# Optimization experiments

Hardware: AMD Instinct MI355X
Metric: run time of the kernel (lower is better)

## Reference

```python
import jax, jax.numpy as jnp
import numpy as np

HEADS, DIM_HEAD = 8, 96
DIM = HEADS * DIM_HEAD            # 768
DEPTH = 8
MEM_LAYERS = (4, 5)               # layers with KNN-retrieval attention
TOPK = 32                         # num_retrieved_memories
CLIP_LEN, PREFIX_LEN = 10, 10
NEG = -1e9


def layernorm(x, g, b):
    m = x.mean(-1, keepdims=True)
    v = ((x - m) ** 2).mean(-1, keepdims=True)
    return (x - m) * jax.lax.rsqrt(v + 1e-5) * g + b


def attention(x, wq_l, wkv_l, wo_l, mem_k=None, mem_v=None):
    # one-headed key/values (memorizing-transformers style), multi-head queries
    b, n, _ = x.shape
    q = (x @ wq_l).reshape(b, n, HEADS, DIM_HEAD).transpose(0, 2, 1, 3)  # [b,h,n,d]
    q = q * (DIM_HEAD ** -0.5)
    kv = x @ wkv_l                                   # [b,n,2d]
    k, v = kv[..., :DIM_HEAD], kv[..., DIM_HEAD:]    # [b,n,d] each
    sim = jnp.einsum('bhid,bjd->bhij', q, k)         # local scores
    causal = jnp.tril(jnp.ones((n, n), dtype=bool))
    sim = jnp.where(causal, sim, NEG)
    if mem_k is not None:
        # exact inner-product top-k retrieval from per-batch memory bank
        mem_sim = jnp.einsum('bhid,bmd->bhim', q, mem_k)      # [b,h,n,M]
        top_sim, top_idx = jax.lax.top_k(mem_sim, TOPK)       # [b,h,n,K]
        mem_v_sel = jnp.take_along_axis(
            mem_v[:, None, None], top_idx[..., None], axis=3)  # [b,h,n,K,d]
        attn = jax.nn.softmax(jnp.concatenate([top_sim, sim], axis=-1), axis=-1)
        mem_attn, loc_attn = attn[..., :TOPK], attn[..., TOPK:]
        out = (jnp.einsum('bhij,bhijd->bhid', mem_attn, mem_v_sel)
               + jnp.einsum('bhij,bjd->bhid', loc_attn, v))
    else:
        attn = jax.nn.softmax(sim, axis=-1)
        out = jnp.einsum('bhij,bjd->bhid', attn, v)
    out = out.transpose(0, 2, 1, 3).reshape(b, n, DIM)
    return out @ wo_l


def setup_inputs() -> dict:
    key = jax.random.key(0)
    ks = jax.random.split(key, 12)
    s = 0.02
    inp = {
        'x': jax.random.normal(ks[0], (16, 640), jnp.float32),
        'linear_w': jax.random.normal(ks[1], (640, CLIP_LEN * DIM), jnp.float32) * s,
        'linear_b': jnp.zeros((CLIP_LEN * DIM,), jnp.float32),
        'prefix_const': jax.random.normal(ks[2], (PREFIX_LEN, DIM), jnp.float32),
        'ln1_g': jnp.ones((DEPTH, DIM), jnp.float32),
        'ln1_b': jnp.zeros((DEPTH, DIM), jnp.float32),
        'wq': jax.random.normal(ks[3], (DEPTH, DIM, DIM), jnp.float32) * s,
        'wkv': jax.random.normal(ks[4], (DEPTH, DIM, 2 * DIM_HEAD), jnp.float32) * s,
        'wo': jax.random.normal(ks[5], (DEPTH, DIM, DIM), jnp.float32) * s,
        'ln2_g': jnp.ones((DEPTH, DIM), jnp.float32),
        'ln2_b': jnp.zeros((DEPTH, DIM), jnp.float32),
        'w1': jax.random.normal(ks[6], (DEPTH, DIM, 4 * DIM), jnp.float32) * s,
        'b1': jnp.zeros((DEPTH, 4 * DIM), jnp.float32),
        'w2': jax.random.normal(ks[7], (DEPTH, 4 * DIM, DIM), jnp.float32) * s,
        'b2': jnp.zeros((DEPTH, DIM), jnp.float32),
        'lnf_g': jnp.ones((DIM,), jnp.float32),
        'lnf_b': jnp.zeros((DIM,), jnp.float32),
        'mem_k': jax.random.normal(ks[8], (16, 32768, DIM_HEAD), jnp.float32),
        'mem_v': jax.random.normal(ks[9], (16, 32768, DIM_HEAD), jnp.float32),
    }
    return inp


def reference(x, linear_w, linear_b, prefix_const,
              ln1_g, ln1_b, wq, wkv, wo, ln2_g, ln2_b,
              w1, b1, w2, b2, lnf_g, lnf_b, mem_k, mem_v):
    b = x.shape[0]
    # linear projection of clip feature -> clip_length tokens
    h = (x @ linear_w + linear_b).reshape(b, CLIP_LEN, DIM)
    prefix = jnp.broadcast_to(prefix_const[None], (b, PREFIX_LEN, DIM))
    t = jnp.concatenate([h, prefix], axis=1)  # [b, 20, dim]
    for l in range(DEPTH):
        mk, mv = (mem_k, mem_v) if l in MEM_LAYERS else (None, None)
        t = t + attention(layernorm(t, ln1_g[l], ln1_b[l]), wq[l], wkv[l], wo[l], mk, mv)
        hf = layernorm(t, ln2_g[l], ln2_b[l])
        t = t + (jax.nn.gelu(hf @ w1[l] + b1[l]) @ w2[l] + b2[l])
    t = layernorm(t, lnf_g, lnf_b)
    return t[:, CLIP_LEN:]  # [b, prefix_length, dim]
```

## Files before the change

### kernel.cpp

```cpp
#include <hip/hip_runtime.h>
#include <hip/hip_bf16.h>

#define BB 16
#define NSEQ 20
#define HEADS 8
#define DH 96
#define DIM 768
#define FF 3072
#define KMEM 32768
#define NCHUNK 8
#define CHUNK 4096
#define CAP 128

typedef unsigned short u16;
typedef __attribute__((ext_vector_type(8))) short short8v;
typedef __attribute__((ext_vector_type(4))) float f32x4;

__device__ __forceinline__ u16 f2bu(float x) {
    __hip_bfloat16 h = __float2bfloat16(x);
    return *reinterpret_cast<u16*>(&h);
}

__global__ __launch_bounds__(256) void conv_k(const float* __restrict__ src, u16* __restrict__ dst, int n)
{
    int i = blockIdx.x * 256 + threadIdx.x;
    if (i < n) dst[i] = f2bu(src[i]);
}

__device__ __forceinline__ void tconv_tile(const float* __restrict__ src, u16* __restrict__ dst,
                                           int K, int N, int kt, int nt, int tx, int ty)
{
    __shared__ float tile[32][33];
    int k0 = kt * 32, n0 = nt * 32;
#pragma unroll
    for (int i = 0; i < 4; i++)
        tile[ty + 8 * i][tx] = src[(size_t)(k0 + ty + 8 * i) * N + n0 + tx];
    __syncthreads();
#pragma unroll
    for (int i = 0; i < 4; i++)
        dst[(size_t)(n0 + ty + 8 * i) * K + k0 + tx] = f2bu(tile[tx][ty + 8 * i]);
}

__global__ __launch_bounds__(256) void tconv_k(const float* __restrict__ src, u16* __restrict__ dst, int K, int N)
{
    int tilesN = N >> 5;
    tconv_tile(src, dst, K, N, blockIdx.x / tilesN, blockIdx.x % tilesN,
               threadIdx.x & 31, threadIdx.x >> 5);
}

__global__ __launch_bounds__(256) void wconv5_k(const float* __restrict__ wq, const float* __restrict__ wkv,
    const float* __restrict__ wo, const float* __restrict__ w1, const float* __restrict__ w2,
    u16* __restrict__ wt)
{
    int bx = blockIdx.x;
    int tx = threadIdx.x & 31, ty = threadIdx.x >> 5;
    if (bx < 576)       tconv_tile(wq,  wt + 0,       768, 768,  bx / 24,          bx % 24,          tx, ty);
    else if (bx < 720)  tconv_tile(wkv, wt + 589824,  768, 192,  (bx - 576) / 6,   (bx - 576) % 6,   tx, ty);
    else if (bx < 1296) tconv_tile(wo,  wt + 737280,  768, 768,  (bx - 720) / 24,  (bx - 720) % 24,  tx, ty);
    else if (bx < 3600) tconv_tile(w1,  wt + 1327104, 768, 3072, (bx - 1296) / 96, (bx - 1296) % 96, tx, ty);
    else                tconv_tile(w2,  wt + 3686400, 3072, 768, (bx - 3600) / 24, (bx - 3600) % 24, tx, ty);
}

__device__ __forceinline__ void storeC(float* C, size_t idx, float v) { C[idx] = v; }
__device__ __forceinline__ void storeC(u16* C, size_t idx, float v)   { C[idx] = f2bu(v); }

template <typename CT>
__global__ __launch_bounds__(256) void gemm_bt(const u16* __restrict__ A, const u16* __restrict__ Bt,
    const float* __restrict__ bias, const float* __restrict__ resid, CT* __restrict__ C,
    int M, int N, int K, int lda, int ldc, float scale, int act)
{
    int tid = threadIdx.x;
    int w = tid >> 6, lane = tid & 63;
    int m0 = blockIdx.y * 16;
    int n0 = blockIdx.x * 128 + w * 32;
    int row = lane & 15;
    int kg  = lane >> 4;
    const u16* arow = A + (size_t)(m0 + row) * lda + kg * 8;
    int c0 = n0 + row;
    int c1 = n0 + 16 + row;
    const u16* bt0 = Bt + (size_t)min(c0, N - 1) * K + kg * 8;
    const u16* bt1 = Bt + (size_t)min(c1, N - 1) * K + kg * 8;
    f32x4 acc0 = {0.f, 0.f, 0.f, 0.f};
    f32x4 acc1 = {0.f, 0.f, 0.f, 0.f};
#pragma unroll 2
    for (int k0 = 0; k0 < K; k0 += 32) {
        short8v af = *(const short8v*)(arow + k0);
        short8v b0 = *(const short8v*)(bt0 + k0);
        short8v b1 = *(const short8v*)(bt1 + k0);
        acc0 = __builtin_amdgcn_mfma_f32_16x16x32_bf16(af, b0, acc0, 0, 0, 0);
        acc1 = __builtin_amdgcn_mfma_f32_16x16x32_bf16(af, b1, acc1, 0, 0, 0);
    }
#pragma unroll
    for (int r = 0; r < 4; r++) {
        int rw = m0 + kg * 4 + r;
        if (c0 < N) {
            float v = acc0[r] * scale;
            if (bias) v += bias[c0];
            if (act) {
                float xx = v;
                float tt = 0.7978845608028654f * (xx + 0.044715f * xx * xx * xx);
                v = 0.5f * xx * (1.0f + tanhf(tt));
            }
            if (resid) v += resid[(size_t)rw * ldc + c0];
            storeC(C, (size_t)rw * ldc + c0, v);
        }
        if (c1 < N) {
            float v = acc1[r] * scale;
            if (bias) v += bias[c1];
            if (act) {
                float xx = v;
                float tt = 0.7978845608028654f * (xx + 0.044715f * xx * xx * xx);
                v = 0.5f * xx * (1.0f + tanhf(tt));
            }
            if (resid) v += resid[(size_t)rw * ldc + c1];
            storeC(C, (size_t)rw * ldc + c1, v);
        }
    }
}

__global__ __launch_bounds__(256) void ln_k(const float* __restrict__ x, const float* __restrict__ g,
    const float* __restrict__ bb, u16* __restrict__ y)
{
    int row = blockIdx.x;
    const float* xr = x + (size_t)row * DIM;
    int tid = threadIdx.x;
    float v0 = xr[tid], v1 = xr[tid + 256], v2 = xr[tid + 512];
    __shared__ float red[4];
    float s = v0 + v1 + v2;
    for (int off = 32; off; off >>= 1) s += __shfl_down(s, off);
    if ((tid & 63) == 0) red[tid >> 6] = s;
    __syncthreads();
    float mean = (red[0] + red[1] + red[2] + red[3]) * (1.f / 768.f);
    __syncthreads();
    float d0 = v0 - mean, d1 = v1 - mean, d2 = v2 - mean;
    s = d0 * d0 + d1 * d1 + d2 * d2;
    for (int off = 32; off; off >>= 1) s += __shfl_down(s, off);
    if ((tid & 63) == 0) red[tid >> 6] = s;
    __syncthreads();
    float var = (red[0] + red[1] + red[2] + red[3]) * (1.f / 768.f);
    float rs = rsqrtf(var + 1e-5f);
    u16* yr = y + (size_t)row * DIM;
    yr[tid]       = f2bu(d0 * rs * g[tid]       + bb[tid]);
    yr[tid + 256] = f2bu(d1 * rs * g[tid + 256] + bb[tid + 256]);
    yr[tid + 512] = f2bu(d2 * rs * g[tid + 512] + bb[tid + 512]);
}

__global__ __launch_bounds__(256) void lnf_k(const float* __restrict__ x, const float* __restrict__ g,
    const float* __restrict__ bb, float* __restrict__ out)
{
    int blk = blockIdx.x;
    int b = blk / 10, ii = blk - b * 10;
    int row = b * NSEQ + 10 + ii;
    const float* xr = x + (size_t)row * DIM;
    int tid = threadIdx.x;
    float v0 = xr[tid], v1 = xr[tid + 256], v2 = xr[tid + 512];
    __shared__ float red[4];
    float s = v0 + v1 + v2;
    for (int off = 32; off; off >>= 1) s += __shfl_down(s, off);
    if ((tid & 63) == 0) red[tid >> 6] = s;
    __syncthreads();
    float mean = (red[0] + red[1] + red[2] + red[3]) * (1.f / 768.f);
    __syncthreads();
    float d0 = v0 - mean, d1 = v1 - mean, d2 = v2 - mean;
    s = d0 * d0 + d1 * d1 + d2 * d2;
    for (int off = 32; off; off >>= 1) s += __shfl_down(s, off);
    if ((tid & 63) == 0) red[tid >> 6] = s;
    __syncthreads();
    float var = (red[0] + red[1] + red[2] + red[3]) * (1.f / 768.f);
    float rs = rsqrtf(var + 1e-5f);
    float* orow = out + ((size_t)(b * 10 + ii)) * DIM;
    orow[tid]       = d0 * rs * g[tid]       + bb[tid];
    orow[tid + 256] = d1 * rs * g[tid + 256] + bb[tid + 256];
    orow[tid + 512] = d2 * rs * g[tid + 512] + bb[tid + 512];
}

__global__ __launch_bounds__(256) void prefix_k(const float* __restrict__ p, float* __restrict__ t)
{
    int idx = blockIdx.x * 256 + threadIdx.x;
    if (idx < BB * 7680) {
        int b = idx / 7680;
        int r = idx - b * 7680;
        t[(size_t)b * (NSEQ * DIM) + 7680 + r] = p[r];
    }
}

__global__ __launch_bounds__(256) void lattn_k(const float* __restrict__ q, const float* __restrict__ kv,
    u16* __restrict__ ao)
{
    int b = blockIdx.x, h = blockIdx.y;
    __shared__ float sims[NSEQ][NSEQ];
    __shared__ float probs[NSEQ][NSEQ];
    const float* qb = q + (size_t)b * NSEQ * DIM + h * DH;
    const float* kb = kv + (size_t)b * NSEQ * 192;
    int tid = threadIdx.x;
    for (int p = tid; p < NSEQ * NSEQ; p += 256) {
        int i = p / NSEQ, j = p - i * NSEQ;
        float s;
        if (j > i) s = -1.0e9f;
        else {
            s = 0.f;
            for (int d = 0; d < DH; d++) s = fmaf(qb[(size_t)i * DIM + d], kb[j * 192 + d], s);
        }
        sims[i][j] = s;
    }
    __syncthreads();
    if (tid < NSEQ) {
        int i = tid;
        float m = -1e30f;
        for (int j = 0; j < NSEQ; j++) m = fmaxf(m, sims[i][j]);
        float sum = 0.f;
        for (int j = 0; j < NSEQ; j++) { float e = expf(sims[i][j] - m); probs[i][j] = e; sum += e; }
        float inv = 1.f / sum;
        for (int j = 0; j < NSEQ; j++) probs[i][j] *= inv;
    }
    __syncthreads();
    for (int p = tid; p < NSEQ * DH; p += 256) {
        int i = p / DH, d = p - i * DH;
        float o = 0.f;
        for (int j = 0; j <= i; j++) o = fmaf(probs[i][j], kb[j * 192 + 96 + d], o);
        ao[((size_t)b * NSEQ + i) * DIM + h * DH + d] = f2bu(o);
    }
}

__device__ __forceinline__ bool tk_better(float va, int ia, float vb, int ib) {
    return (va > vb) || (va == vb && ia < ib);
}

__device__ __forceinline__ void lds_fence() {
    asm volatile("s_waitcnt lgkmcnt(0)" ::: "memory");
    __builtin_amdgcn_sched_barrier(0);
}

__device__ void topk32(float* bv, int* bi, int cnt, int lane,
                       float& ov, int& oi, float& thr_out) {
    lds_fence();
    float v0 = (lane < cnt)      ? bv[lane]      : -3.0e38f;
    int   i0 = (lane < cnt)      ? bi[lane]      : 0x7fffffff;
    float v1 = (lane + 64 < cnt) ? bv[lane + 64] : -3.0e38f;
    int   i1 = (lane + 64 < cnt) ? bi[lane + 64] : 0x7fffffff;
    lds_fence();
#pragma unroll
    for (int k = 2; k <= 128; k <<= 1) {
#pragma unroll
        for (int j = 64; j >= 1; j >>= 1) {
            if (j >= k) continue;
            if (j == 64) {
                bool asc = ((lane & k) == 0);
                bool b01 = tk_better(v0, i0, v1, i1);
                if (b01 != asc) { float tv = v0; int ti = i0; v0 = v1; i0 = i1; v1 = tv; i1 = ti; }
            } else {
                {
                    float pv = __shfl_xor(v0, j); int pi = __shfl_xor(i0, j);
                    bool asc = ((lane & k) == 0);
                    bool first = ((lane & j) == 0);
                    bool mb = tk_better(v0, i0, pv, pi);
                    bool keep = first ? (mb == asc) : (mb != asc);
                    if (!keep) { v0 = pv; i0 = pi; }
                }
                {
                    float pv = __shfl_xor(v1, j); int pi = __shfl_xor(i1, j);
                    bool asc = (((lane + 64) & k) == 0);
                    bool first = ((lane & j) == 0);
                    bool mb = tk_better(v1, i1, pv, pi);
                    bool keep = first ? (mb == asc) : (mb != asc);
                    if (!keep) { v1 = pv; i1 = pi; }
                }
            }
        }
    }
    if (lane < 32) { bv[lane] = v0; bi[lane] = i0; }
    lds_fence();
    ov = v0; oi = i0;
    thr_out = __shfl(v0, 31);
}

__device__ __forceinline__ void tk_pass(const float4 kr[6], const float4 qreg[5][6],
    float thrR[5], int cntR[5], float (*bufv)[CAP], int (*bufi)[CAP],
    int r0, int lane, int qt, int key)
{
    float a[5];
#pragma unroll
    for (int rr = 0; rr < 5; rr++) a[rr] = 0.f;
#pragma unroll
    for (int i = 0; i < 6; i++) {
        float4 kv = kr[i];
#pragma unroll
        for (int rr = 0; rr < 5; rr++) {
            float4 qv = qreg[rr][i];
            a[rr] = fmaf(qv.x, kv.x, a[rr]);
            a[rr] = fmaf(qv.y, kv.y, a[rr]);
            a[rr] = fmaf(qv.z, kv.z, a[rr]);
            a[rr] = fmaf(qv.w, kv.w, a[rr]);
        }
    }
#pragma unroll
    for (int rr = 0; rr < 5; rr++) {
        a[rr] += __shfl_xor(a[rr], 1);
        a[rr] += __shfl_xor(a[rr], 2);
    }
#pragma unroll
    for (int rr = 0; rr < 5; rr++) {
        bool cand = (qt == 0) && (a[rr] >= thrR[rr]);
        unsigned long long mask = __ballot(cand);
        int n = __popcll(mask);
        if (n) {
            int r = r0 + rr;
            if (cntR[rr] + n > CAP) {
                float dv; int di;
                topk32(&bufv[r][0], &bufi[r][0], cntR[rr], lane, dv, di, thrR[rr]);
                cntR[rr] = 32;
            }
            int pos = cntR[rr] + __popcll(mask & ((1ull << lane) - 1ull));
            if (cand) { bufv[r][pos] = a[rr]; bufi[r][pos] = key; }
            cntR[rr] += n;
        }
    }
}

__global__ __launch_bounds__(256, 2) void memtopk_k(const float* __restrict__ q, const float* __restrict__ memk,
    float* __restrict__ tkv, int* __restrict__ tki)
{
    __shared__ float bufv[NSEQ][CAP];
    __shared__ int   bufi[NSEQ][CAP];
    int c = blockIdx.x, h = blockIdx.y, b = blockIdx.z;
    int tid = threadIdx.x;
    int lane = tid & 63;
    int w = tid >> 6;
    int r0 = w * 5;
    int qt = lane & 3;
    int kk = lane >> 2;

    float4 qreg[5][6];
#pragma unroll
    for (int rr = 0; rr < 5; rr++) {
        const float4* qrow = (const float4*)(q + ((size_t)(b * NSEQ + r0 + rr)) * DIM + h * DH + qt * 24);
#pragma unroll
        for (int i = 0; i < 6; i++) qreg[rr][i] = qrow[i];
    }

    float thrR[5]; int cntR[5];
#pragma unroll
    for (int rr = 0; rr < 5; rr++) { thrR[rr] = -3.0e38f; cntR[rr] = 0; }

    const float* kbase = memk + (size_t)b * KMEM * DH;
    int k0 = c * CHUNK;

    float4 ka[6], kb2[6];
    {
        const float4* kp = (const float4*)(kbase + (size_t)(k0 + kk) * DH + qt * 24);
#pragma unroll
        for (int i = 0; i < 6; i++) ka[i] = kp[i];
    }
    for (int p = 0; p < CHUNK / 16; p += 2) {
        int key0 = k0 + p * 16 + kk;
        {
            const float4* kp = (const float4*)(kbase + (size_t)(key0 + 16) * DH + qt * 24);
#pragma unroll
            for (int i = 0; i < 6; i++) kb2[i] = kp[i];
        }
        tk_pass(ka, qreg, thrR, cntR, bufv, bufi, r0, lane, qt, key0);
        if (p + 2 < CHUNK / 16) {
            const float4* kp = (const float4*)(kbase + (size_t)(key0 + 32) * DH + qt * 24);
#pragma unroll
            for (int i = 0; i < 6; i++) ka[i] = kp[i];
        }
        tk_pass(kb2, qreg, thrR, cntR, bufv, bufi, r0, lane, qt, key0 + 16);
    }
#pragma unroll
    for (int rr = 0; rr < 5; rr++) {
        int r = r0 + rr;
        float ov; int oi; float dthr;
        topk32(&bufv[r][0], &bufi[r][0], cntR[rr], lane, ov, oi, dthr);
        if (lane < 32) {
            size_t base = ((((size_t)b * HEADS + h) * NSEQ + r) * NCHUNK + c) * 32;
            tkv[base + lane] = ov;
            tki[base + lane] = oi;
        }
    }
}

__global__ __launch_bounds__(64) void memattn_k(const float* __restrict__ q, const float* __restrict__ kv,
    const float* __restrict__ memv, const float* __restrict__ tkv, const int* __restrict__ tki,
    u16* __restrict__ ao)
{
    int i = blockIdx.x, h = blockIdx.y, b = blockIdx.z;
    __shared__ float cv[NCHUNK * 32];
    __shared__ int   ci[NCHUNK * 32];
    __shared__ float selv[32];
    __shared__ int   seli[32];
    __shared__ float ls[NSEQ];
    __shared__ float probs[52];
    int tid = threadIdx.x;
    size_t base = (((size_t)b * HEADS + h) * NSEQ + i) * (NCHUNK * 32);
#pragma unroll
    for (int s = 0; s < NCHUNK * 32 / 64; s++) {
        cv[tid + 64 * s] = tkv[base + tid + 64 * s];
        ci[tid + 64 * s] = tki[base + tid + 64 * s];
    }
    const float* qr = q + ((size_t)b * NSEQ + i) * DIM + h * DH;
    const float* kvb = kv + (size_t)b * NSEQ * 192;
    if (tid <= i) {
        float s = 0.f;
        for (int d = 0; d < DH; d++) s = fmaf(qr[d], kvb[tid * 192 + d], s);
        ls[tid] = s;
    }
    __syncthreads();
    for (int r = 0; r < 32; r++) {
        float bv = -3.0e38f; int bidx = 0x7fffffff; int bs = 0;
#pragma unroll
        for (int s = 0; s < NCHUNK * 32 / 64; s++) {
            float v = cv[tid + 64 * s]; int ix = ci[tid + 64 * s];
            if (tk_better(v, ix, bv, bidx)) { bv = v; bidx = ix; bs = tid + 64 * s; }
        }
        for (int off = 32; off; off >>= 1) {
            float ovv = __shfl_down(bv, off);
            int oii = __shfl_down(bidx, off);
            int oss = __shfl_down(bs, off);
            if (tk_better(ovv, oii, bv, bidx)) { bv = ovv; bidx = oii; bs = oss; }
        }
        if (tid == 0) { selv[r] = bv; seli[r] = bidx; cv[bs] = -3.0e38f; }
        __syncthreads();
    }
    if (tid == 0) {
        float m = -1e30f;
        for (int r = 0; r < 32; r++) m = fmaxf(m, selv[r]);
        for (int j = 0; j <= i; j++) m = fmaxf(m, ls[j]);
        float sum = 0.f;
        for (int r = 0; r < 32; r++) { float e = expf(selv[r] - m); probs[r] = e; sum += e; }
        for (int j = 0; j <= i; j++) { float e = expf(ls[j] - m); probs[32 + j] = e; sum += e; }
        float inv = 1.f / sum;
        for (int r = 0; r < 32 + i + 1; r++) probs[r] *= inv;
    }
    __syncthreads();
    const float* mvb = memv + (size_t)b * KMEM * DH;
    for (int d = tid; d < DH; d += 64) {
        float o = 0.f;
        for (int r = 0; r < 32; r++) o = fmaf(probs[r], mvb[(size_t)seli[r] * DH + d], o);
        for (int j = 0; j <= i; j++) o = fmaf(probs[32 + j], kvb[j * 192 + 96 + d], o);
        ao[((size_t)b * NSEQ + i) * DIM + h * DH + d] = f2bu(o);
    }
}

extern "C" void kernel_launch(void* const* d_in, const int* in_sizes, int n_in,
                              void* d_out, int out_size, void* d_ws, size_t ws_size,
                              hipStream_t stream) {
    const float* x            = (const float*)d_in[0];
    const float* linear_w     = (const float*)d_in[1];
    const float* linear_b     = (const float*)d_in[2];
    const float* prefix_const = (const float*)d_in[3];
    const float* ln1_g        = (const float*)d_in[4];
    const float* ln1_b        = (const float*)d_in[5];
    const float* wq           = (const float*)d_in[6];
    const float* wkv          = (const float*)d_in[7];
    const float* wo           = (const float*)d_in[8];
    const float* ln2_g        = (const float*)d_in[9];
    const float* ln2_b        = (const float*)d_in[10];
    const float* w1           = (const float*)d_in[11];
    const float* b1           = (const float*)d_in[12];
    const float* w2           = (const float*)d_in[13];
    const float* b2           = (const float*)d_in[14];
    const float* lnf_g        = (const float*)d_in[15];
    const float* lnf_b        = (const float*)d_in[16];
    const float* mem_k        = (const float*)d_in[17];
    const float* mem_v        = (const float*)d_in[18];

    float* ws = (float*)d_ws;
    float* t    = ws;
    u16*   yb   = (u16*)(ws + 245760);
    float* qb   = ws + 491520;
    float* kvb  = ws + 737280;
    u16*   aob  = (u16*)(ws + 798720);
    u16*   h1b  = (u16*)(ws + 1044480);
    float* tkv  = ws + 2027520;
    int*   tki  = (int*)(ws + 2682880);
    u16*   wt   = (u16*)(ws + 3338240);
    u16*   xb   = (u16*)(ws + 6361088);
    float* out  = (float*)d_out;

    const float qscale = 0.10206207261596577f;
    const size_t WQT = 0, WKVT = 589824, WOT = 737280, W1T = 1327104, W2T = 3686400;

    conv_k<<<40, 256, 0, stream>>>(x, xb, 16 * 640);
    tconv_k<<<4800, 256, 0, stream>>>(linear_w, wt, 640, 7680);
    gemm_bt<float><<<dim3(60, 1), 256, 0, stream>>>(xb, wt, linear_b, nullptr, t,
                                                    16, 7680, 640, 640, 15360, 1.f, 0);
    prefix_k<<<dim3(480), 256, 0, stream>>>(prefix_const, t);

    for (int l = 0; l < 8; l++) {
        wconv5_k<<<5904, 256, 0, stream>>>(wq + (size_t)l * DIM * DIM, wkv + (size_t)l * DIM * 192,
                                           wo + (size_t)l * DIM * DIM, w1 + (size_t)l * DIM * FF,
                                           w2 + (size_t)l * FF * DIM, wt);
        ln_k<<<320, 256, 0, stream>>>(t, ln1_g + (size_t)l * DIM, ln1_b + (size_t)l * DIM, yb);
        gemm_bt<float><<<dim3(6, 20), 256, 0, stream>>>(yb, wt + WQT, nullptr, nullptr, qb,
                                                        320, 768, 768, 768, 768, qscale, 0);
        gemm_bt<float><<<dim3(2, 20), 256, 0, stream>>>(yb, wt + WKVT, nullptr, nullptr, kvb,
                                                        320, 192, 768, 768, 192, 1.f, 0);
        if (l == 4 || l == 5) {
            memtopk_k<<<dim3(NCHUNK, HEADS, BB), 256, 0, stream>>>(qb, mem_k, tkv, tki);
            memattn_k<<<dim3(NSEQ, HEADS, BB), 64, 0, stream>>>(qb, kvb, mem_v, tkv, tki, aob);
        } else {
            lattn_k<<<dim3(BB, HEADS), 256, 0, stream>>>(qb, kvb, aob);
        }
        gemm_bt<float><<<dim3(6, 20), 256, 0, stream>>>(aob, wt + WOT, nullptr, t, t,
                                                        320, 768, 768, 768, 768, 1.f, 0);
        ln_k<<<320, 256, 0, stream>>>(t, ln2_g + (size_t)l * DIM, ln2_b + (size_t)l * DIM, yb);
        gemm_bt<u16><<<dim3(24, 20), 256, 0, stream>>>(yb, wt + W1T, b1 + (size_t)l * FF, nullptr, h1b,
                                                       320, 3072, 768, 768, 3072, 1.f, 1);
        gemm_bt<float><<<dim3(6, 20), 256, 0, stream>>>(h1b, wt + W2T, b2 + (size_t)l * DIM, t, t,
                                                        320, 768, 3072, 3072, 768, 1.f, 0);
    }
    lnf_k<<<160, 256, 0, stream>>>(t, lnf_g, lnf_b, out);
}
```

Measured before the change: 2.298 ms.

## Batch all-layer weight conversion, fuse Q/KV GEMMs, and halve topk chunk count

When the workspace is large enough, all eight layers' weights are transposed and converted to bf16 in one launch instead of one launch per layer, giving a larger grid and fewer serialized launches. The Q and KV projections become a single fused MFMA GEMM over 960 output columns, which routes columns to qb or kvb and reduces the launch count. The memory top-k uses 4 chunks of 8192 instead of 8 of 4096, which cuts the candidates to merge but lowers parallelism. Workspace offsets are rearranged to fit the per-layer weight copies, with a fallback to the per-layer path when space is short.

```diff
diff --git a/kernel.cpp b/kernel.cpp
--- a/kernel.cpp
+++ b/kernel.cpp
@@ -8,8 +8,8 @@
 #define DIM 768
 #define FF 3072
 #define KMEM 32768
-#define NCHUNK 8
-#define CHUNK 4096
+#define NCHUNK 4
+#define CHUNK 8192
 #define CAP 128
 
 typedef unsigned short u16;
@@ -48,10 +48,17 @@
                threadIdx.x & 31, threadIdx.x >> 5);
 }
 
-__global__ __launch_bounds__(256) void wconv5_k(const float* __restrict__ wq, const float* __restrict__ wkv,
+__global__ __launch_bounds__(256) void wconv5L_k(const float* __restrict__ wq, const float* __restrict__ wkv,
     const float* __restrict__ wo, const float* __restrict__ w1, const float* __restrict__ w2,
-    u16* __restrict__ wt)
-{
+    u16* __restrict__ wt, size_t wtStride)
+{
+    int l = blockIdx.y;
+    wq += (size_t)l * 589824;
+    wkv += (size_t)l * 147456;
+    wo += (size_t)l * 589824;
+    w1 += (size_t)l * 2359296;
+    w2 += (size_t)l * 2359296;
+    wt += (size_t)l * wtStride;
     int bx = blockIdx.x;
     int tx = threadIdx.x & 31, ty = threadIdx.x >> 5;
     if (bx < 576)       tconv_tile(wq,  wt + 0,       768, 768,  bx / 24,          bx % 24,          tx, ty);
@@ -115,6 +122,41 @@
             if (resid) v += resid[(size_t)rw * ldc + c1];
             storeC(C, (size_t)rw * ldc + c1, v);
         }
+    }
+}
+
+__global__ __launch_bounds__(256) void gemm_qkv(const u16* __restrict__ A, const u16* __restrict__ Bt,
+    float* __restrict__ qb, float* __restrict__ kvb, float qscale)
+{
+    const int N = 960, K = DIM;
+    int tid = threadIdx.x;
+    int w = tid >> 6, lane = tid & 63;
+    int m0 = blockIdx.y * 16;
+    int n0 = blockIdx.x * 128 + w * 32;
+    int row = lane & 15;
+    int kg  = lane >> 4;
+    const u16* arow = A + (size_t)(m0 + row) * K + kg * 8;
+    int c0 = n0 + row;
+    int c1 = n0 + 16 + row;
+    const u16* bt0 = Bt + (size_t)min(c0, N - 1) * K + kg * 8;
+    const u16* bt1 = Bt + (size_t)min(c1, N - 1) * K + kg * 8;
+    f32x4 acc0 = {0.f, 0.f, 0.f, 0.f};
+    f32x4 acc1 = {0.f, 0.f, 0.f, 0.f};
+#pragma unroll 2
+    for (int k0 = 0; k0 < K; k0 += 32) {
+        short8v af = *(const short8v*)(arow + k0);
+        short8v b0 = *(const short8v*)(bt0 + k0);
+        short8v b1 = *(const short8v*)(bt1 + k0);
+        acc0 = __builtin_amdgcn_mfma_f32_16x16x32_bf16(af, b0, acc0, 0, 0, 0);
+        acc1 = __builtin_amdgcn_mfma_f32_16x16x32_bf16(af, b1, acc1, 0, 0, 0);
+    }
+#pragma unroll
+    for (int r = 0; r < 4; r++) {
+        int rw = m0 + kg * 4 + r;
+        if (c0 < 768)      qb[(size_t)rw * 768 + c0] = acc0[r] * qscale;
+        else if (c0 < 960) kvb[(size_t)rw * 192 + (c0 - 768)] = acc0[r];
+        if (c1 < 768)      qb[(size_t)rw * 768 + c1] = acc1[r] * qscale;
+        else if (c1 < 960) kvb[(size_t)rw * 192 + (c1 - 768)] = acc1[r];
     }
 }
 
@@ -472,13 +514,16 @@
     u16*   aob  = (u16*)(ws + 798720);
     u16*   h1b  = (u16*)(ws + 1044480);
     float* tkv  = ws + 2027520;
-    int*   tki  = (int*)(ws + 2682880);
-    u16*   wt   = (u16*)(ws + 3338240);
-    u16*   xb   = (u16*)(ws + 6361088);
+    int*   tki  = (int*)(ws + 2355200);
+    u16*   wt   = (u16*)(ws + 2682880);
     float* out  = (float*)d_out;
 
+    const size_t LAYER_WT = 6045696;
+    const int all8 = (ws_size >= (size_t)(2682880 + 8 * 3022848 + 2560) * 4) ? 1 : 0;
+    u16* xb = (u16*)(ws + (all8 ? (2682880 + 8 * 3022848) : (2682880 + 3022848)));
+
     const float qscale = 0.10206207261596577f;
-    const size_t WQT = 0, WKVT = 589824, WOT = 737280, W1T = 1327104, W2T = 3686400;
+    const size_t WOT = 737280, W1T = 1327104, W2T = 3686400;
 
     conv_k<<<40, 256, 0, stream>>>(x, xb, 16 * 640);
     tconv_k<<<4800, 256, 0, stream>>>(linear_w, wt, 640, 7680);
@@ -486,27 +531,29 @@
                                                     16, 7680, 640, 640, 15360, 1.f, 0);
     prefix_k<<<dim3(480), 256, 0, stream>>>(prefix_const, t);
 
+    if (all8)
+        wconv5L_k<<<dim3(5904, 8), 256, 0, stream>>>(wq, wkv, wo, w1, w2, wt, LAYER_WT);
+
     for (int l = 0; l < 8; l++) {
-        wconv5_k<<<5904, 256, 0, stream>>>(wq + (size_t)l * DIM * DIM, wkv + (size_t)l * DIM * 192,
-                                           wo + (size_t)l * DIM * DIM, w1 + (size_t)l * DIM * FF,
-                                           w2 + (size_t)l * FF * DIM, wt);
+        u16* wtl = wt + (all8 ? (size_t)l * LAYER_WT : 0);
+        if (!all8)
+            wconv5L_k<<<dim3(5904, 1), 256, 0, stream>>>(wq + (size_t)l * 589824, wkv + (size_t)l * 147456,
+                                                         wo + (size_t)l * 589824, w1 + (size_t)l * 2359296,
+                                                         w2 + (size_t)l * 2359296, wtl, 0);
         ln_k<<<320, 256, 0, stream>>>(t, ln1_g + (size_t)l * DIM, ln1_b + (size_t)l * DIM, yb);
-        gemm_bt<float><<<dim3(6, 20), 256, 0, stream>>>(yb, wt + WQT, nullptr, nullptr, qb,
-                                                        320, 768, 768, 768, 768, qscale, 0);
-        gemm_bt<float><<<dim3(2, 20), 256, 0, stream>>>(yb, wt + WKVT, nullptr, nullptr, kvb,
-                                                        320, 192, 768, 768, 192, 1.f, 0);
+        gemm_qkv<<<dim3(8, 20), 256, 0, stream>>>(yb, wtl, qb, kvb, qscale);
         if (l == 4 || l == 5) {
             memtopk_k<<<dim3(NCHUNK, HEADS, BB), 256, 0, stream>>>(qb, mem_k, tkv, tki);
             memattn_k<<<dim3(NSEQ, HEADS, BB), 64, 0, stream>>>(qb, kvb, mem_v, tkv, tki, aob);
         } else {
             lattn_k<<<dim3(BB, HEADS), 256, 0, stream>>>(qb, kvb, aob);
         }
-        gemm_bt<float><<<dim3(6, 20), 256, 0, stream>>>(aob, wt + WOT, nullptr, t, t,
+        gemm_bt<float><<<dim3(6, 20), 256, 0, stream>>>(aob, wtl + WOT, nullptr, t, t,
                                                         320, 768, 768, 768, 768, 1.f, 0);
         ln_k<<<320, 256, 0, stream>>>(t, ln2_g + (size_t)l * DIM, ln2_b + (size_t)l * DIM, yb);
-        gemm_bt<u16><<<dim3(24, 20), 256, 0, stream>>>(yb, wt + W1T, b1 + (size_t)l * FF, nullptr, h1b,
+        gemm_bt<u16><<<dim3(24, 20), 256, 0, stream>>>(yb, wtl + W1T, b1 + (size_t)l * FF, nullptr, h1b,
                                                        320, 3072, 768, 768, 3072, 1.f, 1);
-        gemm_bt<float><<<dim3(6, 20), 256, 0, stream>>>(h1b, wt + W2T, b2 + (size_t)l * DIM, t, t,
+        gemm_bt<float><<<dim3(6, 20), 256, 0, stream>>>(h1b, wtl + W2T, b2 + (size_t)l * DIM, t, t,
                                                         320, 768, 3072, 3072, 768, 1.f, 0);
     }
     lnf_k<<<160, 256, 0, stream>>>(t, lnf_g, lnf_b, out);
```

Measured after the change: 2.078 ms. -9.6%, faster.
